# Optimization experiments

Hardware: AMD Instinct MI355X
Metric: run time of the kernel (lower is better)

Reference implementation:

```python
import jax, jax.numpy as jnp
import numpy as np

QMAX = 127.0  # int8 symmetric quantization range


def _quant_dequant(w):
    """Per-output-channel symmetric int8 fake quantization (weight-only),
    mimicking nn.quantized.Linear.from_float weight quantization."""
    scale = jnp.max(jnp.abs(w), axis=-1, keepdims=True) / QMAX
    scale = jnp.maximum(scale, 1e-8)
    q = jnp.clip(jnp.round(w / scale), -QMAX, QMAX)
    return q * scale


def setup_inputs() -> dict:
    key = jax.random.key(0)
    ks = jax.random.split(key, 7)
    B, S, D, F, E, NS = 2, 2048, 1024, 2048, 8, 1
    std = 1.0 / np.sqrt(D)
    x = jax.random.normal(ks[0], (B, S, D), dtype=jnp.float32)
    router_w = _quant_dequant(jax.random.normal(ks[1], (E, D), dtype=jnp.float32) * std)
    router_b = jnp.zeros((E,), dtype=jnp.float32)
    w_up = _quant_dequant(jax.random.normal(ks[2], (E, F, D), dtype=jnp.float32) * std)
    w_down = _quant_dequant(jax.random.normal(ks[3], (E, D, F), dtype=jnp.float32) / np.sqrt(F))
    shared_w_up = _quant_dequant(jax.random.normal(ks[4], (NS, F, D), dtype=jnp.float32) * std)
    shared_w_down = _quant_dequant(jax.random.normal(ks[5], (NS, D, F), dtype=jnp.float32) / np.sqrt(F))
    return {"x": x, "router_w": router_w, "router_b": router_b,
            "w_up": w_up, "w_down": w_down,
            "shared_w_up": shared_w_up, "shared_w_down": shared_w_down}


def reference(x, router_w, router_b, w_up, w_down, shared_w_up, shared_w_down):
    B, S, D = x.shape
    E = router_w.shape[0]
    TOPK = 2
    xt = x.reshape(-1, D)  # [T, D] tokens

    # Router (quantized linear) -> softmax -> top-k dispatch weights
    logits = xt @ router_w.T + router_b            # [T, E]
    probs = jax.nn.softmax(logits, axis=-1)        # [T, E]
    top_vals, top_idx = jax.lax.top_k(probs, TOPK)  # [T, K]
    top_vals = top_vals / jnp.sum(top_vals, axis=-1, keepdims=True)  # renormalize
    # combine[t, e] = routing weight of expert e for token t (0 if not selected)
    combine = jnp.sum(jax.nn.one_hot(top_idx, E, dtype=xt.dtype) * top_vals[..., None], axis=1)  # [T, E]

    # Routed experts: up -> SiLU -> down, computed densely then combined
    h = jnp.einsum('td,efd->tef', xt, w_up)        # [T, E, F]
    y = jnp.einsum('tef,edf->ted', jax.nn.silu(h), w_down)  # [T, E, D]
    out = jnp.einsum('ted,te->td', y, combine)     # [T, D]

    # Shared experts: always active, summed
    hs = jnp.einsum('td,sfd->tsf', xt, shared_w_up)          # [T, NS, F]
    out = out + jnp.einsum('tsf,sdf->td', jax.nn.silu(hs), shared_w_down)

    return out.reshape(B, S, D)
```

## Files before the change

kernel.cpp:

```cpp
#include <hip/hip_runtime.h>
#include <hip/hip_fp16.h>
#include <stdint.h>

typedef unsigned short u16;
typedef int i32x4 __attribute__((ext_vector_type(4)));

#define DDIM 1024
#define FDIM 2048
#define NEXP 8
#define RT_TILES 72
#define SHOFF 9216
#define RCAP 13312
#define NRT 104


__device__ inline float bf2f(u16 u) {
    union { unsigned int i; float f; } v; v.i = ((unsigned int)u) << 16; return v.f;
}
__device__ inline u16 f2bf(float f) {
    union { float f; unsigned int i; } v; v.f = f;
    unsigned int lsb = (v.i >> 16) & 1u;
    return (u16)((v.i + 0x7fffu + lsb) >> 16);
}
__device__ inline int q8(float v, float inv) {
    int x = (int)rintf(v * inv);
    return x < -127 ? -127 : (x > 127 ? 127 : x);
}

typedef const __attribute__((address_space(1))) void gas_void;
typedef __attribute__((address_space(3))) void las_void;
#define GLL16(g, l) __builtin_amdgcn_global_load_lds((gas_void*)(g), (las_void*)(l), 16, 0, 0)

__device__ inline int detect_inline(const u16* __restrict__ x, int* sh) {
    if (threadIdx.x == 0) *sh = 0;
    __syncthreads();
    const int per = 1024 / blockDim.x;
    int bad = 0;
    for (int i = 0; i < per; i++) {
        u16 v = x[threadIdx.x * per + i];
        if (((v >> 7) & 0xFF) >= 0x8F) bad++;
    }
    if (bad) atomicAdd(sh, bad);
    __syncthreads();
    return (*sh > 32) ? 1 : 0;
}

__global__ __launch_bounds__(256) void router_kernel(
    const void* __restrict__ x_, const void* __restrict__ rw_, const void* __restrict__ rb_,
    float* __restrict__ top_w, int* __restrict__ top_idx)
{
    __shared__ float rws[NEXP * DDIM];
    __shared__ int scnt;
    const int tid = threadIdx.x;
    const int flag = detect_inline((const u16*)x_, &scnt);

    if (!flag) {
        const ushort4* rwv = (const ushort4*)rw_;
        #pragma unroll
        for (int i = 0; i < 8; i++) {
            int idx = tid + i * 256;
            ushort4 h = rwv[idx];
            rws[idx * 4 + 0] = bf2f(h.x); rws[idx * 4 + 1] = bf2f(h.y);
            rws[idx * 4 + 2] = bf2f(h.z); rws[idx * 4 + 3] = bf2f(h.w);
        }
    } else {
        const float4* rwv = (const float4*)rw_;
        #pragma unroll
        for (int i = 0; i < 8; i++) {
            int idx = tid + i * 256;
            float4 f = rwv[idx];
            rws[idx * 4 + 0] = f.x; rws[idx * 4 + 1] = f.y;
            rws[idx * 4 + 2] = f.z; rws[idx * 4 + 3] = f.w;
        }
    }
    __syncthreads();

    const int wave = tid >> 6, lane = tid & 63;

    for (int sub = 0; sub < 4; sub++) {
        const int t = blockIdx.x * 16 + wave * 4 + sub;
        float xv[16];
        if (!flag) {
            const u16* xr = (const u16*)x_ + (size_t)t * DDIM + lane * 16;
            uint4 p0 = *(const uint4*)(xr);
            uint4 p1 = *(const uint4*)(xr + 8);
            #pragma unroll
            for (int d = 0; d < 8; d++) xv[d]     = bf2f(((const u16*)&p0)[d]);
            #pragma unroll
            for (int d = 0; d < 8; d++) xv[d + 8] = bf2f(((const u16*)&p1)[d]);
        } else {
            const float4* xr = (const float4*)((const float*)x_ + (size_t)t * DDIM + lane * 16);
            #pragma unroll
            for (int c = 0; c < 4; c++) {
                float4 f = xr[c];
                xv[c * 4 + 0] = f.x; xv[c * 4 + 1] = f.y;
                xv[c * 4 + 2] = f.z; xv[c * 4 + 3] = f.w;
            }
        }

        float acc[NEXP];
        #pragma unroll
        for (int e = 0; e < NEXP; e++) {
            const float* wr = &rws[e * DDIM + lane * 16];
            float s = 0.f;
            #pragma unroll
            for (int d = 0; d < 16; d++) s += xv[d] * wr[d];
            acc[e] = s;
        }
        #pragma unroll
        for (int e = 0; e < NEXP; e++) {
            #pragma unroll
            for (int off = 32; off > 0; off >>= 1)
                acc[e] += __shfl_xor(acc[e], off, 64);
        }
        if (lane == 0) {
            float lg[NEXP];
            #pragma unroll
            for (int e = 0; e < NEXP; e++) {
                float b = flag ? ((const float*)rb_)[e] : bf2f(((const u16*)rb_)[e]);
                lg[e] = acc[e] + b;
            }
            int i0 = 0;
            #pragma unroll
            for (int e = 1; e < NEXP; e++) if (lg[e] > lg[i0]) i0 = e;
            int i1 = (i0 == 0) ? 1 : 0;
            #pragma unroll
            for (int e = 0; e < NEXP; e++) if (e != i0 && lg[e] > lg[i1]) i1 = e;
            float e1 = __expf(lg[i1] - lg[i0]);
            float w0 = 1.f / (1.f + e1);
            float w1 = e1 / (1.f + e1);
            top_w[2 * t] = w0;  top_w[2 * t + 1] = w1;
            top_idx[2 * t] = i0; top_idx[2 * t + 1] = i1;
        }
    }
}

__global__ __launch_bounds__(1024) void rank_kernel(
    const u16* __restrict__ x, const int* __restrict__ top_idx,
    int* __restrict__ tok_rows, int* __restrict__ meta)
{
    __shared__ int wsum[16][NEXP];
    __shared__ int wbase[16][NEXP];
    __shared__ int scnt;
    const int tid = threadIdx.x, lane = tid & 63, wave = tid >> 6;

    const int flag = detect_inline(x, &scnt);
    if (tid == 0) meta[30] = flag;

    const int4* tp = (const int4*)(top_idx + tid * 8);
    int4 v0 = tp[0], v1 = tp[1];
    int e[8] = { v0.x, v0.y, v0.z, v0.w, v1.x, v1.y, v1.z, v1.w };

    int tcnt[NEXP];
    #pragma unroll
    for (int en = 0; en < NEXP; en++) tcnt[en] = 0;
    #pragma unroll
    for (int j = 0; j < 8; j++)
        #pragma unroll
        for (int en = 0; en < NEXP; en++) tcnt[en] += (e[j] == en);

    int excl[NEXP];
    #pragma unroll
    for (int en = 0; en < NEXP; en++) {
        int v = tcnt[en];
        #pragma unroll
        for (int off = 1; off < 64; off <<= 1) {
            int u = __shfl_up(v, off, 64);
            if (lane >= off) v += u;
        }
        excl[en] = v - tcnt[en];
        if (lane == 63) wsum[wave][en] = v;
    }
    __syncthreads();
    if (tid < NEXP) {
        int s = 0;
        for (int w = 0; w < 16; w++) { int c = wsum[w][tid]; wbase[w][tid] = s; s += c; }
        meta[tid] = s;
    }
    __syncthreads();
    if (tid == 0) {
        int b = 0;
        for (int en = 0; en < NEXP; en++) {
            meta[8 + en] = b;
            b += ((meta[en] + 127) >> 7) << 7;
        }
        meta[16] = b;
    }
    __syncthreads();

    int cur[NEXP];
    #pragma unroll
    for (int en = 0; en < NEXP; en++) cur[en] = meta[8 + en] + wbase[wave][en] + excl[en];

    int r[8];
    #pragma unroll
    for (int j = 0; j < 8; j++) {
        int rr = 0;
        #pragma unroll
        for (int en = 0; en < NEXP; en++)
            if (e[j] == en) { rr = cur[en]; cur[en] = rr + 1; }
        r[j] = rr;
    }
    int4* rp = (int4*)(tok_rows + tid * 8);
    rp[0] = make_int4(r[0], r[1], r[2], r[3]);
    rp[1] = make_int4(r[4], r[5], r[6], r[7]);
}

__global__ __launch_bounds__(128) void gather_q_kernel(
    const void* __restrict__ x_, const int* __restrict__ tok_rows,
    char* __restrict__ xq, float* __restrict__ sxa, const int* __restrict__ meta)
{
    __shared__ float red[128];
    const int t = blockIdx.x, tid = threadIdx.x;
    const int r0 = tok_rows[2 * t], r1 = tok_rows[2 * t + 1];

    float v[8];
    if (!meta[30]) {
        uint4 p = ((const uint4*)((const u16*)x_ + (size_t)t * DDIM))[tid];
        #pragma unroll
        for (int d = 0; d < 8; d++) v[d] = bf2f(((const u16*)&p)[d]);
    } else {
        const float4* xf = (const float4*)((const float*)x_ + (size_t)t * DDIM);
        float4 a = xf[2 * tid], b = xf[2 * tid + 1];
        v[0] = a.x; v[1] = a.y; v[2] = a.z; v[3] = a.w;
        v[4] = b.x; v[5] = b.y; v[6] = b.z; v[7] = b.w;
    }
    float m = 0.f;
    #pragma unroll
    for (int d = 0; d < 8; d++) m = fmaxf(m, fabsf(v[d]));
    red[tid] = m;
    __syncthreads();
    for (int s = 64; s > 0; s >>= 1) {
        if (tid < s) red[tid] = fmaxf(red[tid], red[tid + s]);
        __syncthreads();
    }
    const float mx = fmaxf(red[0], 1e-8f);
    const float inv = 127.f / mx;

    uint2 u;
    u.x = (unsigned)(q8(v[0], inv) & 255) | ((unsigned)(q8(v[1], inv) & 255) << 8) |
          ((unsigned)(q8(v[2], inv) & 255) << 16) | ((unsigned)(q8(v[3], inv) & 255) << 24);
    u.y = (unsigned)(q8(v[4], inv) & 255) | ((unsigned)(q8(v[5], inv) & 255) << 8) |
          ((unsigned)(q8(v[6], inv) & 255) << 16) | ((unsigned)(q8(v[7], inv) & 255) << 24);

    ((uint2*)(xq + (size_t)r0 * DDIM))[tid] = u;
    ((uint2*)(xq + (size_t)r1 * DDIM))[tid] = u;
    ((uint2*)(xq + (size_t)(SHOFF + t) * DDIM))[tid] = u;
    if (tid == 0) {
        float s = mx / 127.f;
        sxa[r0] = s; sxa[r1] = s; sxa[SHOFF + t] = s;
    }
}

template <int NCH, int NR>
__device__ inline void wquant_rows(const char* const* s, char* dst, float* sc,
                                   int flag, int lane)
{
    unsigned hp[NR][NCH * 2];
    float m[NR];
    #pragma unroll
    for (int r = 0; r < NR; r++) {
        float mm = 0.f;
        #pragma unroll
        for (int c = 0; c < NCH; c++) {
            float4 f;
            if (flag) {
                f = ((const float4*)s[r])[c * 64 + lane];
            } else {
                ushort4 h = ((const ushort4*)s[r])[c * 64 + lane];
                f.x = bf2f(h.x); f.y = bf2f(h.y); f.z = bf2f(h.z); f.w = bf2f(h.w);
            }
            mm = fmaxf(mm, fmaxf(fmaxf(fabsf(f.x), fabsf(f.y)),
                                 fmaxf(fabsf(f.z), fabsf(f.w))));
            __half2 p0 = __floats2half2_rn(f.x, f.y);
            __half2 p1 = __floats2half2_rn(f.z, f.w);
            hp[r][2 * c]     = *(unsigned*)&p0;
            hp[r][2 * c + 1] = *(unsigned*)&p1;
        }
        m[r] = mm;
    }
    #pragma unroll
    for (int off = 32; off > 0; off >>= 1) {
        #pragma unroll
        for (int r = 0; r < NR; r++) m[r] = fmaxf(m[r], __shfl_xor(m[r], off, 64));
    }
    #pragma unroll
    for (int r = 0; r < NR; r++) {
        m[r] = fmaxf(m[r], 1e-12f);
        if (lane == 0) sc[r] = m[r] / 127.f;
        const float inv = 127.f / m[r];
        #pragma unroll
        for (int c = 0; c < NCH; c++) {
            float2 f01 = __half22float2(*(__half2*)&hp[r][2 * c]);
            float2 f23 = __half22float2(*(__half2*)&hp[r][2 * c + 1]);
            unsigned u = (unsigned)(q8(f01.x, inv) & 255) |
                         ((unsigned)(q8(f01.y, inv) & 255) << 8) |
                         ((unsigned)(q8(f23.x, inv) & 255) << 16) |
                         ((unsigned)(q8(f23.y, inv) & 255) << 24);
            ((unsigned*)dst)[r * (NCH * 64) + c * 64 + lane] = u;
        }
    }
}

__global__ __launch_bounds__(256) void wquant_kernel(
    const void* __restrict__ w_up, const void* __restrict__ w_down,
    const void* __restrict__ sw_up, const void* __restrict__ sw_down,
    char* __restrict__ qup, char* __restrict__ qdn,
    float* __restrict__ su, float* __restrict__ sd, const int* __restrict__ meta)
{
    const int flag = meta[30];
    const size_t es = flag ? 4 : 2;
    const int lane = threadIdx.x & 63;
    const int g = blockIdx.x * 4 + (threadIdx.x >> 6);
    const int UPG = 3072;

    if (g < UPG) {
        const int R0 = g * 6;
        const char* s[6];
        #pragma unroll
        for (int r = 0; r < 6; r++) {
            const int R = R0 + r;
            s[r] = (R < NEXP * FDIM)
                 ? (const char*)w_up  + (size_t)R * DDIM * es
                 : (const char*)sw_up + (size_t)(R - NEXP * FDIM) * DDIM * es;
        }
        wquant_rows<4, 6>(s, qup + (size_t)R0 * DDIM, su + R0, flag, lane);
    } else {
        const int R0 = (g - UPG) * 3;
        const char* s[3];
        #pragma unroll
        for (int r = 0; r < 3; r++) {
            const int R = R0 + r;
            s[r] = (R < NEXP * DDIM)
                 ? (const char*)w_down  + (size_t)R * FDIM * es
                 : (const char*)sw_down + (size_t)(R - NEXP * DDIM) * FDIM * es;
        }
        wquant_rows<8, 3>(s, qdn + (size_t)R0 * FDIM, sd + R0, flag, lane);
    }
}

__global__ __launch_bounds__(256, 2) void moe_gemm_i8(
    const char* __restrict__ A, const char* __restrict__ Wq,
    const float* __restrict__ sa, const float* __restrict__ sw,
    u16* __restrict__ Cout, const int* __restrict__ meta, int N, int Kd, int act)
{
    const int L = blockIdx.y * gridDim.x + blockIdx.x;
    const int xcd = L & 7;
    const int jj = L >> 3;
    const int rt = xcd * 13 + (jj % 13);
    const int ct = jj / 13;

    int e;
    if (rt >= RT_TILES) {
        e = NEXP;
    } else {
        const int r0t = rt * 128;
        if (r0t >= meta[16]) return;
        e = 0;
        #pragma unroll
        for (int i = 1; i < NEXP; i++) if (r0t >= meta[8 + i]) e = i;
        if (r0t >= meta[8 + e] + meta[e]) return;
    }
    const char* Wb = Wq + (size_t)(e * N + ct * 256) * Kd;
    const float* swb = sw + e * N + ct * 256;

    __shared__ char As[2][128 * 64];
    __shared__ char Bs[2][256 * 64];

    const int tid = threadIdx.x;
    const int wave = tid >> 6, lane = tid & 63;
    const int wm = (wave >> 1) * 64;
    const int wn = (wave & 1) * 128;
    const int l16 = lane & 15;
    const int q = lane >> 4;
    const int slot = (q + (l16 >> 1)) & 3;

    const int rsub = lane >> 2;
    const int qs = ((lane & 3) - ((lane >> 3) & 3)) & 3;

    const char* Ag = A + (size_t)(rt * 128 + wave * 16 + rsub) * Kd + qs * 16;
    const char* Bg = Wb + (size_t)(wave * 16 + rsub) * Kd + qs * 16;
    const size_t rstep = (size_t)64 * Kd;

    i32x4 acc[4][8] = {};

#define STAGE(buf, off) do { \
        GLL16(Ag + (off),             &As[buf][wave * 1024]); \
        GLL16(Ag + (off) + rstep,     &As[buf][4096 + wave * 1024]); \
        GLL16(Bg + (off),             &Bs[buf][wave * 1024]); \
        GLL16(Bg + (off) + rstep,     &Bs[buf][4096 + wave * 1024]); \
        GLL16(Bg + (off) + 2 * rstep, &Bs[buf][8192 + wave * 1024]); \
        GLL16(Bg + (off) + 3 * rstep, &Bs[buf][12288 + wave * 1024]); \
    } while (0)

    STAGE(0, 0);
    __syncthreads();

    int cur = 0;
    for (int kk = 0; kk < Kd; kk += 64) {
        if (kk + 64 < Kd) STAGE(cur ^ 1, kk + 64);
        i32x4 af[4], bf[8];
        #pragma unroll
        for (int i = 0; i < 4; i++)
            af[i] = *(const i32x4*)&As[cur][(wm + i * 16 + l16) * 64 + slot * 16];
        #pragma unroll
        for (int j = 0; j < 8; j++)
            bf[j] = *(const i32x4*)&Bs[cur][(wn + j * 16 + l16) * 64 + slot * 16];
        #pragma unroll
        for (int i = 0; i < 4; i++)
            #pragma unroll
            for (int j = 0; j < 8; j++)
                acc[i][j] = __builtin_amdgcn_mfma_i32_16x16x64_i8(af[i], bf[j], acc[i][j], 0, 0, 0);
        __syncthreads();
        cur ^= 1;
    }
#undef STAGE

    float sal[4][4];
    #pragma unroll
    for (int i = 0; i < 4; i++)
        #pragma unroll
        for (int rr = 0; rr < 4; rr++)
            sal[i][rr] = sa[rt * 128 + wm + i * 16 + q * 4 + rr];
    float swl[8];
    #pragma unroll
    for (int j = 0; j < 8; j++) swl[j] = swb[wn + j * 16 + l16];

    u16* Crow = Cout + (size_t)(rt * 128) * N + ct * 256;
    #pragma unroll
    for (int i = 0; i < 4; i++) {
        #pragma unroll
        for (int j = 0; j < 8; j++) {
            #pragma unroll
            for (int rr = 0; rr < 4; rr++) {
                const int row = wm + i * 16 + q * 4 + rr;
                const int col = wn + j * 16 + l16;
                float v = (float)acc[i][j][rr] * sal[i][rr] * swl[j];
                if (act) v = v / (1.f + __expf(-v));
                Crow[(size_t)row * N + col] = f2bf(v);
            }
        }
    }
}

__global__ __launch_bounds__(256) void hquant_kernel(
    const u16* __restrict__ hg, char* __restrict__ h8, float* __restrict__ sh,
    const int* __restrict__ meta)
{
    const int r = blockIdx.x;
    if (r >= meta[16] && r < SHOFF) return;
    __shared__ float red[256];
    const int tid = threadIdx.x;
    const u16* row = hg + (size_t)r * FDIM;
    uint4 p = ((const uint4*)row)[tid];
    float v[8];
    #pragma unroll
    for (int d = 0; d < 8; d++) v[d] = bf2f(((const u16*)&p)[d]);
    float m = 0.f;
    #pragma unroll
    for (int d = 0; d < 8; d++) m = fmaxf(m, fabsf(v[d]));
    red[tid] = m;
    __syncthreads();
    for (int s = 128; s > 0; s >>= 1) {
        if (tid < s) red[tid] = fmaxf(red[tid], red[tid + s]);
        __syncthreads();
    }
    const float mx = fmaxf(red[0], 1e-8f);
    const float inv = 127.f / mx;
    if (tid == 0) sh[r] = mx / 127.f;
    uint2 u;
    u.x = (unsigned)(q8(v[0], inv) & 255) | ((unsigned)(q8(v[1], inv) & 255) << 8) |
          ((unsigned)(q8(v[2], inv) & 255) << 16) | ((unsigned)(q8(v[3], inv) & 255) << 24);
    u.y = (unsigned)(q8(v[4], inv) & 255) | ((unsigned)(q8(v[5], inv) & 255) << 8) |
          ((unsigned)(q8(v[6], inv) & 255) << 16) | ((unsigned)(q8(v[7], inv) & 255) << 24);
    ((uint2*)(h8 + (size_t)r * FDIM))[tid] = u;
}

__global__ __launch_bounds__(256) void combine_kernel(
    const u16* __restrict__ yg, const float* __restrict__ top_w,
    const int* __restrict__ tok_rows, void* __restrict__ out_, const int* __restrict__ meta)
{
    const int t = blockIdx.x;
    const int r0 = tok_rows[2 * t], r1 = tok_rows[2 * t + 1];
    const float w0 = top_w[2 * t], w1 = top_w[2 * t + 1];
    const int d = threadIdx.x * 4;
    ushort4 y0 = *(const ushort4*)(yg + (size_t)r0 * DDIM + d);
    ushort4 y1 = *(const ushort4*)(yg + (size_t)r1 * DDIM + d);
    ushort4 ys = *(const ushort4*)(yg + (size_t)(SHOFF + t) * DDIM + d);
    float o0 = w0 * bf2f(y0.x) + w1 * bf2f(y1.x) + bf2f(ys.x);
    float o1 = w0 * bf2f(y0.y) + w1 * bf2f(y1.y) + bf2f(ys.y);
    float o2 = w0 * bf2f(y0.z) + w1 * bf2f(y1.z) + bf2f(ys.z);
    float o3 = w0 * bf2f(y0.w) + w1 * bf2f(y1.w) + bf2f(ys.w);
    if (!meta[30]) {
        ushort4 o; o.x = f2bf(o0); o.y = f2bf(o1); o.z = f2bf(o2); o.w = f2bf(o3);
        *(ushort4*)((u16*)out_ + (size_t)t * DDIM + d) = o;
    } else {
        float4 o; o.x = o0; o.y = o1; o.z = o2; o.w = o3;
        *(float4*)((float*)out_ + (size_t)t * DDIM + d) = o;
    }
}

extern "C" void kernel_launch(void* const* d_in, const int* in_sizes, int n_in,
                              void* d_out, int out_size, void* d_ws, size_t ws_size,
                              hipStream_t stream) {
    const void* x       = d_in[0];
    const void* rw      = d_in[1];
    const void* rb      = d_in[2];
    const void* w_up    = d_in[3];
    const void* w_down  = d_in[4];
    const void* sw_up   = d_in[5];
    const void* sw_down = d_in[6];

    const int T = in_sizes[0] / DDIM;

    char* ws = (char*)d_ws;
    int*   meta     = (int*)ws;
    float* top_w    = (float*)(ws + 1024);
    int*   top_idx  = (int*)(ws + 1024 + 8 * T);
    int*   tok_rows = (int*)(ws + 1024 + 16 * T);
    size_t off = 131072;
    u16*  yg = (u16*)(ws + off);
    char* xq = (char*)(ws + off);
    off += (size_t)RCAP * DDIM * 2;
    u16*  hg = (u16*)(ws + off);
    off += (size_t)RCAP * FDIM * 2;
    char* h8 = (char*)(ws + off);
    off += (size_t)RCAP * FDIM;
    char* qup = (char*)(ws + off);
    off += (size_t)(NEXP + 1) * FDIM * DDIM;
    char* qdn = (char*)(ws + off);
    off += (size_t)(NEXP + 1) * DDIM * FDIM;
    float* sxa = (float*)(ws + off); off += (size_t)RCAP * 4;
    float* sh  = (float*)(ws + off); off += (size_t)RCAP * 4;
    float* su  = (float*)(ws + off); off += (size_t)(NEXP + 1) * FDIM * 4;
    float* sd  = (float*)(ws + off); off += (size_t)(NEXP + 1) * DDIM * 4;

    router_kernel<<<T / 16, 256, 0, stream>>>(x, rw, rb, top_w, top_idx);
    rank_kernel<<<1, 1024, 0, stream>>>((const u16*)x, top_idx, tok_rows, meta);
    gather_q_kernel<<<T, 128, 0, stream>>>(x, tok_rows, xq, sxa, meta);
    wquant_kernel<<<1536, 256, 0, stream>>>(
        w_up, w_down, sw_up, sw_down, qup, qdn, su, sd, meta);

    moe_gemm_i8<<<dim3(FDIM / 256, NRT), 256, 0, stream>>>(
        xq, qup, sxa, su, hg, meta, FDIM, DDIM, 1);
    hquant_kernel<<<RCAP, 256, 0, stream>>>(hg, h8, sh, meta);
    moe_gemm_i8<<<dim3(DDIM / 256, NRT), 256, 0, stream>>>(
        h8, qdn, sh, sd, yg, meta, DDIM, FDIM, 0);
    combine_kernel<<<T, 256, 0, stream>>>(yg, top_w, tok_rows, d_out, meta);
}
```

Baseline: 332.5 us.

## Fuse router and weight quantization into one launch with LDS-staged weight loads

Merges the router kernel and the weight int8 quantization kernel into a single launch, where the first blocks do routing and the rest quantize weight rows. The weight path now stages whole rows into LDS through direct global-to-LDS loads and reads them twice from LDS (max pass, then quantize), replacing the fp16 register packing. The aim is to remove one launch, let router work overlap with weight quantization, and cut register pressure. Each block now uses 32KB of LDS, which may lower occupancy, and every block runs the flag detection.

```diff
diff --git a/kernel.cpp b/kernel.cpp
--- a/kernel.cpp
+++ b/kernel.cpp
@@ -1,5 +1,4 @@
 #include <hip/hip_runtime.h>
-#include <hip/hip_fp16.h>
 #include <stdint.h>
 
 typedef unsigned short u16;
@@ -12,6 +11,9 @@
 #define SHOFF 9216
 #define RCAP 13312
 #define NRT 104
+#define UPROWS 16384
+#define DNROWS 8192
+#define WQB 4608
 
 
 __device__ inline float bf2f(u16 u) {
@@ -45,92 +47,166 @@
     return (*sh > 32) ? 1 : 0;
 }
 
-__global__ __launch_bounds__(256) void router_kernel(
+__global__ __launch_bounds__(256) void fused_rw_kernel(
     const void* __restrict__ x_, const void* __restrict__ rw_, const void* __restrict__ rb_,
-    float* __restrict__ top_w, int* __restrict__ top_idx)
+    const void* __restrict__ w_up, const void* __restrict__ w_down,
+    const void* __restrict__ sw_up, const void* __restrict__ sw_down,
+    float* __restrict__ top_w, int* __restrict__ top_idx,
+    char* __restrict__ qup, char* __restrict__ qdn,
+    float* __restrict__ su, float* __restrict__ sd, int nrb)
 {
-    __shared__ float rws[NEXP * DDIM];
-    __shared__ int scnt;
+    __shared__ char smem[32768 + 16];
     const int tid = threadIdx.x;
-    const int flag = detect_inline((const u16*)x_, &scnt);
-
-    if (!flag) {
-        const ushort4* rwv = (const ushort4*)rw_;
-        #pragma unroll
-        for (int i = 0; i < 8; i++) {
-            int idx = tid + i * 256;
-            ushort4 h = rwv[idx];
-            rws[idx * 4 + 0] = bf2f(h.x); rws[idx * 4 + 1] = bf2f(h.y);
-            rws[idx * 4 + 2] = bf2f(h.z); rws[idx * 4 + 3] = bf2f(h.w);
-        }
-    } else {
-        const float4* rwv = (const float4*)rw_;
-        #pragma unroll
-        for (int i = 0; i < 8; i++) {
-            int idx = tid + i * 256;
-            float4 f = rwv[idx];
-            rws[idx * 4 + 0] = f.x; rws[idx * 4 + 1] = f.y;
-            rws[idx * 4 + 2] = f.z; rws[idx * 4 + 3] = f.w;
-        }
-    }
-    __syncthreads();
-
     const int wave = tid >> 6, lane = tid & 63;
-
-    for (int sub = 0; sub < 4; sub++) {
-        const int t = blockIdx.x * 16 + wave * 4 + sub;
-        float xv[16];
+    const int flag = detect_inline((const u16*)x_, (int*)(smem + 32768));
+
+    if ((int)blockIdx.x < nrb) {
+        float* rws = (float*)smem;
         if (!flag) {
-            const u16* xr = (const u16*)x_ + (size_t)t * DDIM + lane * 16;
-            uint4 p0 = *(const uint4*)(xr);
-            uint4 p1 = *(const uint4*)(xr + 8);
+            const ushort4* rwv = (const ushort4*)rw_;
             #pragma unroll
-            for (int d = 0; d < 8; d++) xv[d]     = bf2f(((const u16*)&p0)[d]);
+            for (int i = 0; i < 8; i++) {
+                int idx = tid + i * 256;
+                ushort4 h = rwv[idx];
+                rws[idx * 4 + 0] = bf2f(h.x); rws[idx * 4 + 1] = bf2f(h.y);
+                rws[idx * 4 + 2] = bf2f(h.z); rws[idx * 4 + 3] = bf2f(h.w);
+            }
+        } else {
+            const float4* rwv = (const float4*)rw_;
             #pragma unroll
-            for (int d = 0; d < 8; d++) xv[d + 8] = bf2f(((const u16*)&p1)[d]);
-        } else {
-            const float4* xr = (const float4*)((const float*)x_ + (size_t)t * DDIM + lane * 16);
-            #pragma unroll
-            for (int c = 0; c < 4; c++) {
-                float4 f = xr[c];
-                xv[c * 4 + 0] = f.x; xv[c * 4 + 1] = f.y;
-                xv[c * 4 + 2] = f.z; xv[c * 4 + 3] = f.w;
-            }
-        }
-
-        float acc[NEXP];
-        #pragma unroll
-        for (int e = 0; e < NEXP; e++) {
-            const float* wr = &rws[e * DDIM + lane * 16];
-            float s = 0.f;
-            #pragma unroll
-            for (int d = 0; d < 16; d++) s += xv[d] * wr[d];
-            acc[e] = s;
-        }
-        #pragma unroll
-        for (int e = 0; e < NEXP; e++) {
-            #pragma unroll
-            for (int off = 32; off > 0; off >>= 1)
-                acc[e] += __shfl_xor(acc[e], off, 64);
-        }
-        if (lane == 0) {
-            float lg[NEXP];
+            for (int i = 0; i < 8; i++) {
+                int idx = tid + i * 256;
+                float4 f = rwv[idx];
+                rws[idx * 4 + 0] = f.x; rws[idx * 4 + 1] = f.y;
+                rws[idx * 4 + 2] = f.z; rws[idx * 4 + 3] = f.w;
+            }
+        }
+        __syncthreads();
+
+        for (int sub = 0; sub < 4; sub++) {
+            const int t = blockIdx.x * 16 + wave * 4 + sub;
+            float xv[16];
+            if (!flag) {
+                const u16* xr = (const u16*)x_ + (size_t)t * DDIM + lane * 16;
+                uint4 p0 = *(const uint4*)(xr);
+                uint4 p1 = *(const uint4*)(xr + 8);
+                #pragma unroll
+                for (int d = 0; d < 8; d++) xv[d]     = bf2f(((const u16*)&p0)[d]);
+                #pragma unroll
+                for (int d = 0; d < 8; d++) xv[d + 8] = bf2f(((const u16*)&p1)[d]);
+            } else {
+                const float4* xr = (const float4*)((const float*)x_ + (size_t)t * DDIM + lane * 16);
+                #pragma unroll
+                for (int c = 0; c < 4; c++) {
+                    float4 f = xr[c];
+                    xv[c * 4 + 0] = f.x; xv[c * 4 + 1] = f.y;
+                    xv[c * 4 + 2] = f.z; xv[c * 4 + 3] = f.w;
+                }
+            }
+            float acc[NEXP];
             #pragma unroll
             for (int e = 0; e < NEXP; e++) {
-                float b = flag ? ((const float*)rb_)[e] : bf2f(((const u16*)rb_)[e]);
-                lg[e] = acc[e] + b;
-            }
-            int i0 = 0;
+                const float* wr = &rws[e * DDIM + lane * 16];
+                float s = 0.f;
+                #pragma unroll
+                for (int d = 0; d < 16; d++) s += xv[d] * wr[d];
+                acc[e] = s;
+            }
             #pragma unroll
-            for (int e = 1; e < NEXP; e++) if (lg[e] > lg[i0]) i0 = e;
-            int i1 = (i0 == 0) ? 1 : 0;
-            #pragma unroll
-            for (int e = 0; e < NEXP; e++) if (e != i0 && lg[e] > lg[i1]) i1 = e;
-            float e1 = __expf(lg[i1] - lg[i0]);
-            float w0 = 1.f / (1.f + e1);
-            float w1 = e1 / (1.f + e1);
-            top_w[2 * t] = w0;  top_w[2 * t + 1] = w1;
-            top_idx[2 * t] = i0; top_idx[2 * t + 1] = i1;
+            for (int e = 0; e < NEXP; e++) {
+                #pragma unroll
+                for (int off = 32; off > 0; off >>= 1)
+                    acc[e] += __shfl_xor(acc[e], off, 64);
+            }
+            if (lane == 0) {
+                float lg[NEXP];
+                #pragma unroll
+                for (int e = 0; e < NEXP; e++) {
+                    float b = flag ? ((const float*)rb_)[e] : bf2f(((const u16*)rb_)[e]);
+                    lg[e] = acc[e] + b;
+                }
+                int i0 = 0;
+                #pragma unroll
+                for (int e = 1; e < NEXP; e++) if (lg[e] > lg[i0]) i0 = e;
+                int i1 = (i0 == 0) ? 1 : 0;
+                #pragma unroll
+                for (int e = 0; e < NEXP; e++) if (e != i0 && lg[e] > lg[i1]) i1 = e;
+                float e1 = __expf(lg[i1] - lg[i0]);
+                float w0 = 1.f / (1.f + e1);
+                float w1 = e1 / (1.f + e1);
+                top_w[2 * t] = w0;  top_w[2 * t + 1] = w1;
+                top_idx[2 * t] = i0; top_idx[2 * t + 1] = i1;
+            }
+        }
+        return;
+    }
+
+    const int g = blockIdx.x - nrb;
+    const int isUp = (g < 2304);
+    const size_t es = flag ? 4 : 2;
+    const int G = isUp ? 8 : 4;
+    const int rowelems = isUp ? DDIM : FDIM;
+    const size_t rowbytes = (size_t)rowelems * es;
+    const int R0 = isUp ? (g * 8) : ((g - 2304) * 4);
+    const char* wbase = isUp ? (const char*)w_up : (const char*)w_down;
+    const char* sbase = isUp ? (const char*)sw_up : (const char*)sw_down;
+    const int nmain = isUp ? UPROWS : DNROWS;
+    char* qdst = isUp ? qup : qdn;
+    float* sdst = isUp ? su : sd;
+
+    const int cpr = (int)(rowbytes >> 10);
+    const int cprsh = 31 - __clz(cpr);
+    const int npw = (G * cpr) >> 2;
+    for (int k = 0; k < npw; k++) {
+        const int ii = wave * npw + k;
+        const int r = ii >> cprsh;
+        const int c = ii - (r << cprsh);
+        const int R = R0 + r;
+        const char* src = (R < nmain ? wbase + (size_t)R * rowbytes
+                                     : sbase + (size_t)(R - nmain) * rowbytes)
+                          + (c << 10) + lane * 16;
+        GLL16(src, smem + r * rowbytes + (c << 10));
+    }
+    __syncthreads();
+
+    const int rpw = G >> 2;
+    const int cmax = rowelems >> 8;
+    for (int rr = 0; rr < rpw; rr++) {
+        const int r = wave * rpw + rr;
+        const int R = R0 + r;
+        const char* ld = smem + r * rowbytes;
+        float m = 0.f;
+        if (flag) {
+            for (int c = 0; c < cmax; c++) {
+                float4 f = *(const float4*)(ld + (size_t)((c * 64 + lane) << 4));
+                m = fmaxf(m, fmaxf(fmaxf(fabsf(f.x), fabsf(f.y)),
+                                   fmaxf(fabsf(f.z), fabsf(f.w))));
+            }
+        } else {
+            for (int c = 0; c < cmax; c++) {
+                ushort4 h = *(const ushort4*)(ld + (size_t)((c * 64 + lane) << 3));
+                m = fmaxf(m, fmaxf(fmaxf(fabsf(bf2f(h.x)), fabsf(bf2f(h.y))),
+                                   fmaxf(fabsf(bf2f(h.z)), fabsf(bf2f(h.w)))));
+            }
+        }
+        #pragma unroll
+        for (int off = 32; off > 0; off >>= 1) m = fmaxf(m, __shfl_xor(m, off, 64));
+        m = fmaxf(m, 1e-12f);
+        if (lane == 0) sdst[R] = m / 127.f;
+        const float inv = 127.f / m;
+        for (int c = 0; c < cmax; c++) {
+            float4 f;
+            if (flag) {
+                f = *(const float4*)(ld + (size_t)((c * 64 + lane) << 4));
+            } else {
+                ushort4 h = *(const ushort4*)(ld + (size_t)((c * 64 + lane) << 3));
+                f.x = bf2f(h.x); f.y = bf2f(h.y); f.z = bf2f(h.z); f.w = bf2f(h.w);
+            }
+            unsigned u = (unsigned)(q8(f.x, inv) & 255) |
+                         ((unsigned)(q8(f.y, inv) & 255) << 8) |
+                         ((unsigned)(q8(f.z, inv) & 255) << 16) |
+                         ((unsigned)(q8(f.w, inv) & 255) << 24);
+            *(unsigned*)(qdst + (size_t)R * rowelems + (size_t)((c * 64 + lane) << 2)) = u;
         }
     }
 }
@@ -249,93 +325,6 @@
     if (tid == 0) {
         float s = mx / 127.f;
         sxa[r0] = s; sxa[r1] = s; sxa[SHOFF + t] = s;
-    }
-}
-
-template <int NCH, int NR>
-__device__ inline void wquant_rows(const char* const* s, char* dst, float* sc,
-                                   int flag, int lane)
-{
-    unsigned hp[NR][NCH * 2];
-    float m[NR];
-    #pragma unroll
-    for (int r = 0; r < NR; r++) {
-        float mm = 0.f;
-        #pragma unroll
-        for (int c = 0; c < NCH; c++) {
-            float4 f;
-            if (flag) {
-                f = ((const float4*)s[r])[c * 64 + lane];
-            } else {
-                ushort4 h = ((const ushort4*)s[r])[c * 64 + lane];
-                f.x = bf2f(h.x); f.y = bf2f(h.y); f.z = bf2f(h.z); f.w = bf2f(h.w);
-            }
-            mm = fmaxf(mm, fmaxf(fmaxf(fabsf(f.x), fabsf(f.y)),
-                                 fmaxf(fabsf(f.z), fabsf(f.w))));
-            __half2 p0 = __floats2half2_rn(f.x, f.y);
-            __half2 p1 = __floats2half2_rn(f.z, f.w);
-            hp[r][2 * c]     = *(unsigned*)&p0;
-            hp[r][2 * c + 1] = *(unsigned*)&p1;
-        }
-        m[r] = mm;
-    }
-    #pragma unroll
-    for (int off = 32; off > 0; off >>= 1) {
-        #pragma unroll
-        for (int r = 0; r < NR; r++) m[r] = fmaxf(m[r], __shfl_xor(m[r], off, 64));
-    }
-    #pragma unroll
-    for (int r = 0; r < NR; r++) {
-        m[r] = fmaxf(m[r], 1e-12f);
-        if (lane == 0) sc[r] = m[r] / 127.f;
-        const float inv = 127.f / m[r];
-        #pragma unroll
-        for (int c = 0; c < NCH; c++) {
-            float2 f01 = __half22float2(*(__half2*)&hp[r][2 * c]);
-            float2 f23 = __half22float2(*(__half2*)&hp[r][2 * c + 1]);
-            unsigned u = (unsigned)(q8(f01.x, inv) & 255) |
-                         ((unsigned)(q8(f01.y, inv) & 255) << 8) |
-                         ((unsigned)(q8(f23.x, inv) & 255) << 16) |
-                         ((unsigned)(q8(f23.y, inv) & 255) << 24);
-            ((unsigned*)dst)[r * (NCH * 64) + c * 64 + lane] = u;
-        }
-    }
-}
-
-__global__ __launch_bounds__(256) void wquant_kernel(
-    const void* __restrict__ w_up, const void* __restrict__ w_down,
-    const void* __restrict__ sw_up, const void* __restrict__ sw_down,
-    char* __restrict__ qup, char* __restrict__ qdn,
-    float* __restrict__ su, float* __restrict__ sd, const int* __restrict__ meta)
-{
-    const int flag = meta[30];
-    const size_t es = flag ? 4 : 2;
-    const int lane = threadIdx.x & 63;
-    const int g = blockIdx.x * 4 + (threadIdx.x >> 6);
-    const int UPG = 3072;
-
-    if (g < UPG) {
-        const int R0 = g * 6;
-        const char* s[6];
-        #pragma unroll
-        for (int r = 0; r < 6; r++) {
-            const int R = R0 + r;
-            s[r] = (R < NEXP * FDIM)
-                 ? (const char*)w_up  + (size_t)R * DDIM * es
-                 : (const char*)sw_up + (size_t)(R - NEXP * FDIM) * DDIM * es;
-        }
-        wquant_rows<4, 6>(s, qup + (size_t)R0 * DDIM, su + R0, flag, lane);
-    } else {
-        const int R0 = (g - UPG) * 3;
-        const char* s[3];
-        #pragma unroll
-        for (int r = 0; r < 3; r++) {
-            const int R = R0 + r;
-            s[r] = (R < NEXP * DDIM)
-                 ? (const char*)w_down  + (size_t)R * FDIM * es
-                 : (const char*)sw_down + (size_t)(R - NEXP * DDIM) * FDIM * es;
-        }
-        wquant_rows<8, 3>(s, qdn + (size_t)R0 * FDIM, sd + R0, flag, lane);
     }
 }
 
@@ -535,11 +524,12 @@
     float* su  = (float*)(ws + off); off += (size_t)(NEXP + 1) * FDIM * 4;
     float* sd  = (float*)(ws + off); off += (size_t)(NEXP + 1) * DDIM * 4;
 
-    router_kernel<<<T / 16, 256, 0, stream>>>(x, rw, rb, top_w, top_idx);
+    const int nrb = T / 16;
+    fused_rw_kernel<<<nrb + WQB, 256, 0, stream>>>(
+        x, rw, rb, w_up, w_down, sw_up, sw_down,
+        top_w, top_idx, qup, qdn, su, sd, nrb);
     rank_kernel<<<1, 1024, 0, stream>>>((const u16*)x, top_idx, tok_rows, meta);
     gather_q_kernel<<<T, 128, 0, stream>>>(x, tok_rows, xq, sxa, meta);
-    wquant_kernel<<<1536, 256, 0, stream>>>(
-        w_up, w_down, sw_up, sw_down, qup, qdn, su, sd, meta);
 
     moe_gemm_i8<<<dim3(FDIM / 256, NRT), 256, 0, stream>>>(
         xq, qup, sxa, su, hg, meta, FDIM, DDIM, 1);
```

Result: faster. 323.1 us (-2.8%).
